# Kernel optimization log

Measured on AMD Instinct MI355X. Metric: run time of the kernel, lower is better.

The kernel has to match this reference:

```python
import jax, jax.numpy as jnp
import numpy as np

N, E, M = 50000, 50000, 640000
IN_DIM, D, L = 256, 128, 3

def setup_inputs() -> dict:
    key = jax.random.key(0)
    ks = jax.random.split(key, 8)
    x = jax.random.normal(ks[0], (N, IN_DIM), dtype=jnp.float32)
    hyperedge_index = jax.random.randint(ks[1], (2, M), 0, N, dtype=jnp.int64)
    weightMatrix = jax.random.uniform(ks[2], (E,), dtype=jnp.float32)
    edgesWeights = jax.random.uniform(ks[3], (M,), dtype=jnp.float32)
    stdv_fc = 1.0 / np.sqrt(IN_DIM)
    fc_w = jax.random.uniform(ks[4], (IN_DIM, D), minval=-stdv_fc, maxval=stdv_fc, dtype=jnp.float32)
    fc_b = jax.random.uniform(ks[5], (D,), minval=-stdv_fc, maxval=stdv_fc, dtype=jnp.float32)
    stdv = 1.0 / np.sqrt(D)
    conv_w = jax.random.uniform(ks[6], (L, D, D), minval=-stdv, maxval=stdv, dtype=jnp.float32)
    conv_b = jax.random.uniform(ks[7], (L, D), minval=-stdv, maxval=stdv, dtype=jnp.float32)
    return {"x": x, "hyperedge_index": hyperedge_index, "weightMatrix": weightMatrix,
            "edgesWeights": edgesWeights, "fc_w": fc_w, "fc_b": fc_b,
            "conv_w": conv_w, "conv_b": conv_b}

def reference(x, hyperedge_index, weightMatrix, edgesWeights, fc_w, fc_b, conv_w, conv_b):
    row, col = hyperedge_index[0], hyperedge_index[1]
    n_nodes, n_edges = x.shape[0], weightMatrix.shape[0]
    # degree normalization (computed once, shared by all layers since inputs identical)
    node_deg = jax.ops.segment_sum(weightMatrix[col], row, num_segments=n_nodes) + 1e-8
    hyper_deg = jax.ops.segment_sum(edgesWeights, col, num_segments=n_edges) + 1e-8
    nd = node_deg ** -0.5
    nd = jnp.where(jnp.isinf(nd), 0.0, nd)
    hd = hyper_deg ** -0.5
    hd = jnp.where(jnp.isinf(hd), 0.0, hd)
    norm = hd[col] * nd[row]  # [M]
    h = jax.nn.relu(x @ fc_w + fc_b)  # [N, D]; dropout inactive (eval)
    for i in range(conv_w.shape[0]):
        xt = h @ conv_w[i] + conv_b[i]                                  # [N, D]
        wx = xt[row] * (edgesWeights * norm)[:, None]                   # [M, D]
        hyper_feat = jax.ops.segment_sum(wx, col, num_segments=n_edges)  # [E, D]
        wh = hyper_feat[col] * (weightMatrix[col] * edgesWeights * norm)[:, None]  # [M, D]
        z = jax.ops.segment_sum(wh, row, num_segments=n_nodes)           # [N, D]
        h = jax.nn.relu(h + z)
    return h
```

## Files before the change

kernel.cpp:

```cpp
#include <hip/hip_runtime.h>
#include <hip/hip_bf16.h>
#include <stdint.h>

typedef __attribute__((ext_vector_type(4))) float f4;
typedef __attribute__((ext_vector_type(2))) float f2;
typedef __attribute__((ext_vector_type(2))) int i2;
typedef __attribute__((ext_vector_type(8))) unsigned short us8;
typedef __attribute__((ext_vector_type(4))) unsigned short us4;
typedef __attribute__((ext_vector_type(2))) unsigned short us2;
typedef __attribute__((ext_vector_type(8))) short s8b;
typedef __attribute__((ext_vector_type(4))) float f32x4;

#define CW_SHIFT 8
#define CW (1 << CW_SHIFT)
#define CH 2048

__device__ __forceinline__ float bf2f(unsigned short u) {
  union { unsigned int i; float f; } t; t.i = ((unsigned int)u) << 16; return t.f;
}
__device__ __forceinline__ unsigned short f2bf(float f) {
  union { float f; unsigned int i; } t; t.f = f;
  unsigned int u = t.i;
  return (unsigned short)((u + 0x7FFFu + ((u >> 16) & 1u)) >> 16);
}
__device__ __forceinline__ float cvtload(const void* p, int i, int f16) {
  return f16 ? bf2f(((const unsigned short*)p)[i]) : ((const float*)p)[i];
}

__global__ void detect_kernel(const unsigned int* __restrict__ xb,
                              const unsigned int* __restrict__ ib,
                              int* __restrict__ flags) {
  if (threadIdx.x == 0) {
    int cnt = 0;
    for (int i = 0; i < 256; ++i) {
      unsigned int e = (xb[i] >> 7) & 0xffu;
      if (e >= 110u && e <= 135u) ++cnt;
    }
    flags[0] = (cnt >= 180) ? 1 : 0;
    int zc = 0;
    for (int i = 0; i < 128; ++i) if (ib[2 * i + 1] == 0u) ++zc;
    flags[1] = (zc >= 120) ? 1 : 0;
  }
}

__global__ void cvt_params(const void* __restrict__ wM, const void* __restrict__ fcw,
                           const void* __restrict__ fcb, const void* __restrict__ cw,
                           const void* __restrict__ cb,
                           float* __restrict__ WMf, unsigned short* __restrict__ FCWT,
                           float* __restrict__ FCB, unsigned short* __restrict__ CWT,
                           float* __restrict__ CBf,
                           int E, int L, const int* __restrict__ flags) {
  const int IN_DIM = 256, D = 128;
  int i = blockIdx.x * 256 + threadIdx.x;
  const int f16 = flags[0];
  if (i < E) { WMf[i] = cvtload(wM, i, f16); return; }
  i -= E;
  if (i < IN_DIM * D) {
    int c = i >> 8, k = i & 255;
    FCWT[i] = f2bf(cvtload(fcw, k * D + c, f16));
    return;
  }
  i -= IN_DIM * D;
  if (i < D) { FCB[i] = cvtload(fcb, i, f16); return; }
  i -= D;
  if (i < L * D * D) {
    int l = i >> 14, rem = i & 16383;
    int c = rem >> 7, k = rem & 127;
    CWT[i] = f2bf(cvtload(cw, l * D * D + k * D + c, f16));
    return;
  }
  i -= L * D * D;
  if (i < L * D) CBf[i] = cvtload(cb, i, f16);
}

__global__ __launch_bounds__(256) void bin_count(
    const void* __restrict__ hei, int M, int* __restrict__ cntAB,
    int nbE, int nbN, int nblk, const int* __restrict__ flags) {
  __shared__ int hA[256];
  __shared__ int hB[256];
  const int tid = threadIdx.x, blk = blockIdx.x;
  hA[tid] = 0; hB[tid] = 0;
  __syncthreads();
  const int i64 = flags[1];
  const int mEnd = min(M, (blk + 1) * CH);
  for (int m = blk * CH + tid; m < mEnd; m += 256) {
    int r, c;
    if (i64) {
      r = (int)((const long long*)hei)[m];
      c = (int)((const long long*)hei)[M + m];
    } else {
      r = ((const int*)hei)[m];
      c = ((const int*)hei)[M + m];
    }
    atomicAdd(&hA[c >> CW_SHIFT], 1);
    atomicAdd(&hB[r >> CW_SHIFT], 1);
  }
  __syncthreads();
  if (tid < nbE) cntAB[tid * nblk + blk] = hA[tid];
  if (tid < nbN) cntAB[(nbE + tid) * nblk + blk] = hB[tid];
}

__global__ __launch_bounds__(512) void scanA(int* __restrict__ cnt,
                                             int* __restrict__ btot, int nblk) {
  __shared__ int sc[512];
  const int tid = threadIdx.x, b = blockIdx.x;
  int v = (tid < nblk) ? cnt[b * nblk + tid] : 0;
  sc[tid] = v;
  __syncthreads();
  for (int s = 1; s < 512; s <<= 1) {
    int t = (tid >= s) ? sc[tid - s] : 0;
    __syncthreads();
    sc[tid] += t;
    __syncthreads();
  }
  if (tid < nblk) cnt[b * nblk + tid] = sc[tid] - v;
  if (tid == 511) btot[b] = sc[511];
}

__global__ __launch_bounds__(512) void scanB(const int* __restrict__ btot,
                                             int* __restrict__ bbaseA,
                                             int* __restrict__ bbaseB,
                                             int nbE, int nbN) {
  __shared__ int sc[512];
  const int tid = threadIdx.x;
  const int nb = blockIdx.x ? nbN : nbE;
  const int* src = blockIdx.x ? (btot + nbE) : btot;
  int* dst = blockIdx.x ? bbaseB : bbaseA;
  int v = (tid < nb) ? src[tid] : 0;
  sc[tid] = v;
  __syncthreads();
  for (int s = 1; s < 512; s <<= 1) {
    int t = (tid >= s) ? sc[tid - s] : 0;
    __syncthreads();
    sc[tid] += t;
    __syncthreads();
  }
  if (tid < nb) dst[tid] = sc[tid] - v;
  if (tid == 511) dst[nb] = sc[511];
}

__global__ __launch_bounds__(256) void binscatter(
    const void* __restrict__ hei, const void* __restrict__ ew, int M,
    const int* __restrict__ cntAB,
    const int* __restrict__ bbaseA, const int* __restrict__ bbaseB,
    i2* __restrict__ PAYA, i2* __restrict__ PAYB,
    int nbE, int nbN, int nblk, const int* __restrict__ flags) {
  __shared__ int baseA[256];
  __shared__ int baseB[256];
  const int tid = threadIdx.x, blk = blockIdx.x;
  if (tid < nbE) baseA[tid] = bbaseA[tid] + cntAB[tid * nblk + blk];
  if (tid < nbN) baseB[tid] = bbaseB[tid] + cntAB[(nbE + tid) * nblk + blk];
  __syncthreads();
  const int i64 = flags[1], f16 = flags[0];
  const int mEnd = min(M, (blk + 1) * CH);
  for (int m = blk * CH + tid; m < mEnd; m += 256) {
    int r, c;
    if (i64) {
      r = (int)((const long long*)hei)[m];
      c = (int)((const long long*)hei)[M + m];
    } else {
      r = ((const int*)hei)[m];
      c = ((const int*)hei)[M + m];
    }
    int e = __float_as_int(f16 ? bf2f(((const unsigned short*)ew)[m])
                               : ((const float*)ew)[m]);
    int pA = atomicAdd(&baseA[c >> CW_SHIFT], 1);
    i2 ea; ea[0] = r | ((c & (CW - 1)) << 20); ea[1] = e;
    PAYA[pA] = ea;
    int pB = atomicAdd(&baseB[r >> CW_SHIFT], 1);
    i2 eb; eb[0] = c | ((r & (CW - 1)) << 20); eb[1] = e;
    PAYB[pB] = eb;
  }
}

__global__ __launch_bounds__(256) void finalize3(
    const i2* __restrict__ PAYA, const int* __restrict__ bbaseA,
    i2* __restrict__ ENTA, int* __restrict__ offE, int E,
    const i2* __restrict__ PAYB, const int* __restrict__ bbaseB,
    i2* __restrict__ ENTB, int* __restrict__ offN, int Nn,
    const float* __restrict__ WMf, float* __restrict__ SCE,
    float* __restrict__ ND, int nbE) {
  __shared__ int cnt[CW];
  __shared__ int sc[CW];
  __shared__ int cur[CW];
  __shared__ float fsum[CW];
  int b = blockIdx.x;
  const i2* PAY; const int* bbase; i2* ENT; int* off;
  int nseg, modeB; float* outScale;
  if (b < nbE) {
    PAY = PAYA; bbase = bbaseA; ENT = ENTA; off = offE;
    nseg = E; modeB = 0; outScale = SCE;
  } else {
    b -= nbE;
    PAY = PAYB; bbase = bbaseB; ENT = ENTB; off = offN;
    nseg = Nn; modeB = 1; outScale = ND;
  }
  const int tid = threadIdx.x;
  const int bs = bbase[b], be = bbase[b + 1];
  const int cb = b << CW_SHIFT;
  const int cw = min(CW, nseg - cb);
  for (int i = tid; i < CW; i += 256) { cnt[i] = 0; fsum[i] = 0.f; }
  __syncthreads();
  for (int k = bs + tid; k < be; k += 256)
    atomicAdd(&cnt[(PAY[k][0] >> 20) & (CW - 1)], 1);
  __syncthreads();
  for (int i = tid; i < CW; i += 256) sc[i] = cnt[i];
  __syncthreads();
  for (int s = 1; s < CW; s <<= 1) {
    int t = (tid >= s) ? sc[tid - s] : 0;
    __syncthreads();
    sc[tid] += t;
    __syncthreads();
  }
  {
    int start = bs + sc[tid] - cnt[tid];
    cur[tid] = start;
    if (tid < cw) off[cb + tid] = start;
  }
  if (tid == 0 && b == ((nseg + CW - 1) >> CW_SHIFT) - 1) off[nseg] = be;
  __syncthreads();
  for (int k = bs + tid; k < be; k += 256) {
    i2 p = PAY[k];
    int key = (p[0] >> 20) & (CW - 1);
    int src = p[0] & 0xFFFFF;
    int pos = atomicAdd(&cur[key], 1);
    i2 outp; outp[0] = src; outp[1] = p[1];
    ENT[pos] = outp;
    float add = modeB ? WMf[src] : __int_as_float(p[1]);
    atomicAdd(&fsum[key], add);
  }
  __syncthreads();
  if (tid < cw) {
    float s = fsum[tid] + 1e-8f;
    outScale[cb + tid] = modeB ? rsqrtf(s) : (WMf[cb + tid] / s);
  }
}

template<int KS>
__global__ __launch_bounds__(256) void gemm_mfma3(
    const void* __restrict__ Aptr, const unsigned short* __restrict__ Wt,
    const float* __restrict__ bias, unsigned short* __restrict__ out,
    int Nrows, const int* __restrict__ flags, int relu,
    const float* __restrict__ rowScale) {
  constexpr int K = KS * 32;
  constexpr int KC = K / 8;
  extern __shared__ unsigned short Bs[];
  const int tid = threadIdx.x;
  const int wv = tid >> 6, ln = tid & 63;
  const int lr = ln & 15;
  const int lk = (ln >> 4) << 3;
  const int rowBase = blockIdx.x * 128 + wv * 32;
  const int aF32 = flags ? (flags[0] ? 0 : 1) : 0;

  int ar[2];
#pragma unroll
  for (int t = 0; t < 2; ++t) {
    int r = rowBase + t * 16 + lr;
    ar[t] = (r < Nrows) ? r : (Nrows - 1);
  }

  s8b aR[2][KS];
  if (!aF32) {
#pragma unroll
    for (int t = 0; t < 2; ++t)
#pragma unroll
      for (int ks = 0; ks < KS; ++ks)
        aR[t][ks] = *reinterpret_cast<const s8b*>(
            (const unsigned short*)Aptr + (size_t)ar[t] * K + ks * 32 + lk);
  } else {
#pragma unroll
    for (int t = 0; t < 2; ++t)
#pragma unroll
      for (int ks = 0; ks < KS; ++ks) {
        const float* ap = (const float*)Aptr + (size_t)ar[t] * K + ks * 32 + lk;
        f4 u0 = *reinterpret_cast<const f4*>(ap);
        f4 u1 = *reinterpret_cast<const f4*>(ap + 4);
#pragma unroll
        for (int j = 0; j < 4; ++j) {
          aR[t][ks][j]     = (short)f2bf(u0[j]);
          aR[t][ks][4 + j] = (short)f2bf(u1[j]);
        }
      }
  }

#pragma unroll
  for (int it = 0; it < (128 * KC + 255) / 256; ++it) {
    int ch = it * 256 + tid;
    if (ch < 128 * KC) {
      int row = ch / KC, kc = (ch % KC) << 3;
      us8 v = *reinterpret_cast<const us8*>(Wt + (size_t)row * K + kc);
      int byte = ((row * K + kc) << 1) ^ ((row & 7) << 4);
      *reinterpret_cast<us8*>((char*)Bs + byte) = v;
    }
  }
  __syncthreads();

  f32x4 acc[2][8];
#pragma unroll
  for (int t = 0; t < 2; ++t)
#pragma unroll
    for (int n = 0; n < 8; ++n) acc[t][n] = (f32x4)0.f;

#pragma unroll
  for (int ks = 0; ks < KS; ++ks) {
#pragma unroll
    for (int n = 0; n < 8; ++n) {
      const int brow = n * 16 + lr;
      int byte = ((brow * K + ks * 32 + lk) << 1) ^ ((brow & 7) << 4);
      s8b b = *reinterpret_cast<const s8b*>((const char*)Bs + byte);
      acc[0][n] = __builtin_amdgcn_mfma_f32_16x16x32_bf16(aR[0][ks], b, acc[0][n], 0, 0, 0);
      acc[1][n] = __builtin_amdgcn_mfma_f32_16x16x32_bf16(aR[1][ks], b, acc[1][n], 0, 0, 0);
    }
  }

#pragma unroll
  for (int t = 0; t < 2; ++t) {
    const int orow0 = rowBase + t * 16 + ((ln >> 4) << 2);
#pragma unroll
    for (int n = 0; n < 8; ++n) {
      const int col = n * 16 + lr;
      const float bv = bias[col];
#pragma unroll
      for (int r = 0; r < 4; ++r) {
        int row = orow0 + r;
        if (row >= Nrows) continue;
        float s = acc[t][n][r] + bv;
        if (relu) s = fmaxf(s, 0.f);
        if (rowScale) s *= rowScale[row];
        out[(size_t)row * 128 + col] = f2bf(s);
      }
    }
  }
}

__global__ __launch_bounds__(256) void gather_edge3(
    const int* __restrict__ off, const i2* __restrict__ ENT,
    const float* __restrict__ sc_e, const unsigned short* __restrict__ X,
    unsigned short* __restrict__ out, int nseg) {
  int seg = blockIdx.x * 16 + (threadIdx.x >> 4);
  if (seg >= nseg) return;
  int d = (threadIdx.x & 15) << 3;
  int k0 = off[seg], k1 = off[seg + 1];
  float a0 = 0.f, a1 = 0.f, a2 = 0.f, a3 = 0.f, a4 = 0.f, a5 = 0.f, a6 = 0.f, a7 = 0.f;
  int k = k0;
  for (; k + 4 <= k1; k += 4) {
    i2 e0 = ENT[k], e1 = ENT[k + 1], e2 = ENT[k + 2], e3 = ENT[k + 3];
    us8 v0 = *reinterpret_cast<const us8*>(X + (size_t)e0[0] * 128 + d);
    us8 v1 = *reinterpret_cast<const us8*>(X + (size_t)e1[0] * 128 + d);
    us8 v2 = *reinterpret_cast<const us8*>(X + (size_t)e2[0] * 128 + d);
    us8 v3 = *reinterpret_cast<const us8*>(X + (size_t)e3[0] * 128 + d);
    float c0 = __int_as_float(e0[1]), c1 = __int_as_float(e1[1]);
    float c2 = __int_as_float(e2[1]), c3 = __int_as_float(e3[1]);
    a0 += c0 * bf2f(v0[0]); a1 += c0 * bf2f(v0[1]); a2 += c0 * bf2f(v0[2]); a3 += c0 * bf2f(v0[3]);
    a4 += c0 * bf2f(v0[4]); a5 += c0 * bf2f(v0[5]); a6 += c0 * bf2f(v0[6]); a7 += c0 * bf2f(v0[7]);
    a0 += c1 * bf2f(v1[0]); a1 += c1 * bf2f(v1[1]); a2 += c1 * bf2f(v1[2]); a3 += c1 * bf2f(v1[3]);
    a4 += c1 * bf2f(v1[4]); a5 += c1 * bf2f(v1[5]); a6 += c1 * bf2f(v1[6]); a7 += c1 * bf2f(v1[7]);
    a0 += c2 * bf2f(v2[0]); a1 += c2 * bf2f(v2[1]); a2 += c2 * bf2f(v2[2]); a3 += c2 * bf2f(v2[3]);
    a4 += c2 * bf2f(v2[4]); a5 += c2 * bf2f(v2[5]); a6 += c2 * bf2f(v2[6]); a7 += c2 * bf2f(v2[7]);
    a0 += c3 * bf2f(v3[0]); a1 += c3 * bf2f(v3[1]); a2 += c3 * bf2f(v3[2]); a3 += c3 * bf2f(v3[3]);
    a4 += c3 * bf2f(v3[4]); a5 += c3 * bf2f(v3[5]); a6 += c3 * bf2f(v3[6]); a7 += c3 * bf2f(v3[7]);
  }
  for (; k < k1; ++k) {
    i2 e = ENT[k];
    us8 v = *reinterpret_cast<const us8*>(X + (size_t)e[0] * 128 + d);
    float c = __int_as_float(e[1]);
    a0 += c * bf2f(v[0]); a1 += c * bf2f(v[1]); a2 += c * bf2f(v[2]); a3 += c * bf2f(v[3]);
    a4 += c * bf2f(v[4]); a5 += c * bf2f(v[5]); a6 += c * bf2f(v[6]); a7 += c * bf2f(v[7]);
  }
  float sc = sc_e[seg];
  us8 o;
  o[0] = f2bf(sc * a0); o[1] = f2bf(sc * a1); o[2] = f2bf(sc * a2); o[3] = f2bf(sc * a3);
  o[4] = f2bf(sc * a4); o[5] = f2bf(sc * a5); o[6] = f2bf(sc * a6); o[7] = f2bf(sc * a7);
  *reinterpret_cast<us8*>(out + (size_t)seg * 128 + d) = o;
}

__global__ __launch_bounds__(256) void gather_node3(
    const int* __restrict__ off, const i2* __restrict__ ENT,
    const float* __restrict__ nd, const unsigned short* __restrict__ HF,
    const unsigned short* __restrict__ H, void* __restrict__ out,
    int nseg, int outF32) {
  int seg = blockIdx.x * 16 + (threadIdx.x >> 4);
  if (seg >= nseg) return;
  int d = (threadIdx.x & 15) << 3;
  int k0 = off[seg], k1 = off[seg + 1];
  float a0 = 0.f, a1 = 0.f, a2 = 0.f, a3 = 0.f, a4 = 0.f, a5 = 0.f, a6 = 0.f, a7 = 0.f;
  int k = k0;
  for (; k + 4 <= k1; k += 4) {
    i2 e0 = ENT[k], e1 = ENT[k + 1], e2 = ENT[k + 2], e3 = ENT[k + 3];
    us8 v0 = *reinterpret_cast<const us8*>(HF + (size_t)e0[0] * 128 + d);
    us8 v1 = *reinterpret_cast<const us8*>(HF + (size_t)e1[0] * 128 + d);
    us8 v2 = *reinterpret_cast<const us8*>(HF + (size_t)e2[0] * 128 + d);
    us8 v3 = *reinterpret_cast<const us8*>(HF + (size_t)e3[0] * 128 + d);
    float c0 = __int_as_float(e0[1]), c1 = __int_as_float(e1[1]);
    float c2 = __int_as_float(e2[1]), c3 = __int_as_float(e3[1]);
    a0 += c0 * bf2f(v0[0]); a1 += c0 * bf2f(v0[1]); a2 += c0 * bf2f(v0[2]); a3 += c0 * bf2f(v0[3]);
    a4 += c0 * bf2f(v0[4]); a5 += c0 * bf2f(v0[5]); a6 += c0 * bf2f(v0[6]); a7 += c0 * bf2f(v0[7]);
    a0 += c1 * bf2f(v1[0]); a1 += c1 * bf2f(v1[1]); a2 += c1 * bf2f(v1[2]); a3 += c1 * bf2f(v1[3]);
    a4 += c1 * bf2f(v1[4]); a5 += c1 * bf2f(v1[5]); a6 += c1 * bf2f(v1[6]); a7 += c1 * bf2f(v1[7]);
    a0 += c2 * bf2f(v2[0]); a1 += c2 * bf2f(v2[1]); a2 += c2 * bf2f(v2[2]); a3 += c2 * bf2f(v2[3]);
    a4 += c2 * bf2f(v2[4]); a5 += c2 * bf2f(v2[5]); a6 += c2 * bf2f(v2[6]); a7 += c2 * bf2f(v2[7]);
    a0 += c3 * bf2f(v3[0]); a1 += c3 * bf2f(v3[1]); a2 += c3 * bf2f(v3[2]); a3 += c3 * bf2f(v3[3]);
    a4 += c3 * bf2f(v3[4]); a5 += c3 * bf2f(v3[5]); a6 += c3 * bf2f(v3[6]); a7 += c3 * bf2f(v3[7]);
  }
  for (; k < k1; ++k) {
    i2 e = ENT[k];
    us8 v = *reinterpret_cast<const us8*>(HF + (size_t)e[0] * 128 + d);
    float c = __int_as_float(e[1]);
    a0 += c * bf2f(v[0]); a1 += c * bf2f(v[1]); a2 += c * bf2f(v[2]); a3 += c * bf2f(v[3]);
    a4 += c * bf2f(v[4]); a5 += c * bf2f(v[5]); a6 += c * bf2f(v[6]); a7 += c * bf2f(v[7]);
  }
  float s = nd[seg];
  us8 h = *reinterpret_cast<const us8*>(H + (size_t)seg * 128 + d);
  float r0 = fmaxf(bf2f(h[0]) + s * a0, 0.f);
  float r1 = fmaxf(bf2f(h[1]) + s * a1, 0.f);
  float r2 = fmaxf(bf2f(h[2]) + s * a2, 0.f);
  float r3 = fmaxf(bf2f(h[3]) + s * a3, 0.f);
  float r4 = fmaxf(bf2f(h[4]) + s * a4, 0.f);
  float r5 = fmaxf(bf2f(h[5]) + s * a5, 0.f);
  float r6 = fmaxf(bf2f(h[6]) + s * a6, 0.f);
  float r7 = fmaxf(bf2f(h[7]) + s * a7, 0.f);
  if (outF32) {
    float* op = (float*)out + (size_t)seg * 128 + d;
    f4 o0, o1;
    o0[0] = r0; o0[1] = r1; o0[2] = r2; o0[3] = r3;
    o1[0] = r4; o1[1] = r5; o1[2] = r6; o1[3] = r7;
    *reinterpret_cast<f4*>(op) = o0;
    *reinterpret_cast<f4*>(op + 4) = o1;
  } else {
    us8 o;
    o[0] = f2bf(r0); o[1] = f2bf(r1); o[2] = f2bf(r2); o[3] = f2bf(r3);
    o[4] = f2bf(r4); o[5] = f2bf(r5); o[6] = f2bf(r6); o[7] = f2bf(r7);
    *reinterpret_cast<us8*>((unsigned short*)out + (size_t)seg * 128 + d) = o;
  }
}

extern "C" void kernel_launch(void* const* d_in, const int* in_sizes, int n_in,
                              void* d_out, int out_size, void* d_ws, size_t ws_size,
                              hipStream_t stream) {
  const void* x   = d_in[0];
  const void* hei = d_in[1];
  const void* wM  = d_in[2];
  const void* ew  = d_in[3];
  const void* fcw = d_in[4];
  const void* fcb = d_in[5];
  const void* cw  = d_in[6];
  const void* cb  = d_in[7];

  const int IN_DIM = 256, D = 128;
  const int N = in_sizes[0] / IN_DIM;
  const int M = in_sizes[1] / 2;
  const int E = in_sizes[2];
  const int L = in_sizes[6] / (D * D);

  const int nbE = (E + CW - 1) >> CW_SHIFT;
  const int nbN = (N + CW - 1) >> CW_SHIFT;
  const int nbT = nbE + nbN;
  const int nblk = (M + CH - 1) / CH;

  float* w = (float*)d_ws;
  size_t o = 0;
  auto alloc = [&](size_t n) { float* p = w + o; o += (n + 3) & ~(size_t)3; return p; };

  float* R = alloc((size_t)(N + E) * D / 2);
  unsigned short* XT = (unsigned short*)R;
  unsigned short* HF = XT + (size_t)N * D;
  i2*  PAYA = (i2*)R;
  i2*  PAYB = PAYA + M;

  unsigned short* H  = (unsigned short*)alloc((size_t)N * D / 2);
  i2*    ENTA = (i2*)alloc((size_t)M * 2);
  i2*    ENTB = (i2*)alloc((size_t)M * 2);
  int*   cntAB = (int*)alloc((size_t)nbT * nblk);
  int*   btotAB = (int*)alloc(nbT + 2);
  int*   bbaseA = (int*)alloc(nbE + 2);
  int*   bbaseB = (int*)alloc(nbN + 2);
  float* ND   = alloc(N);
  float* SCE  = alloc(E);
  int*   offE = (int*)alloc(E + 1);
  int*   offN = (int*)alloc(N + 1);
  float* WMf  = alloc(E);
  unsigned short* FCWT = (unsigned short*)alloc((size_t)IN_DIM * D / 2);
  float* FCB  = alloc(D);
  unsigned short* CWT = (unsigned short*)alloc((size_t)L * D * D / 2);
  float* CBf  = alloc((size_t)L * D);
  int*   FLAGS = (int*)alloc(16);

  detect_kernel<<<1, 64, 0, stream>>>((const unsigned int*)x, (const unsigned int*)hei, FLAGS);

  bin_count<<<nblk, 256, 0, stream>>>(hei, M, cntAB, nbE, nbN, nblk, FLAGS);
  {
    int ntot = E + IN_DIM * D + D + L * D * D + L * D;
    cvt_params<<<(ntot + 255) / 256, 256, 0, stream>>>(wM, fcw, fcb, cw, cb,
                                                       WMf, FCWT, FCB, CWT, CBf,
                                                       E, L, FLAGS);
  }

  scanA<<<nbT, 512, 0, stream>>>(cntAB, btotAB, nblk);
  scanB<<<2, 512, 0, stream>>>(btotAB, bbaseA, bbaseB, nbE, nbN);

  binscatter<<<nblk, 256, 0, stream>>>(hei, ew, M, cntAB, bbaseA, bbaseB,
                                       PAYA, PAYB, nbE, nbN, nblk, FLAGS);

  finalize3<<<nbT, 256, 0, stream>>>(PAYA, bbaseA, ENTA, offE, E,
                                     PAYB, bbaseB, ENTB, offN, N,
                                     WMf, SCE, ND, nbE);

  gemm_mfma3<8><<<(N + 127) / 128, 256, 128 * 256 * 2, stream>>>(
      x, FCWT, FCB, H, N, FLAGS, 1, nullptr);

  int segBlkE = (E + 15) / 16, segBlkN = (N + 15) / 16;
  for (int l = 0; l < L; ++l) {
    gemm_mfma3<4><<<(N + 127) / 128, 256, 128 * 128 * 2, stream>>>(
        H, CWT + (size_t)l * D * D, CBf + (size_t)l * D, XT, N,
        (const int*)nullptr, 0, ND);
    gather_edge3<<<segBlkE, 256, 0, stream>>>(offE, ENTA, SCE, XT, HF, E);
    gather_node3<<<segBlkN, 256, 0, stream>>>(
        offN, ENTB, ND, HF, H,
        (l == L - 1) ? d_out : (void*)H, N, (l == L - 1) ? 1 : 0);
  }
}
```

Before: 307.5 us.

## Fuse edge binning into single pass with atomic bucket cursors and fixed-capacity slots

Replaces the count/scan/scatter sequence for bucketing edges with one kernel that stages edges in shared memory, reserves space per bucket via global atomics, and writes into fixed-capacity slot arrays. A small scan then computes compact bucket offsets for finalize. This drops two kernel launches and a second read of the index arrays, at the cost of assuming no bucket exceeds 8192 entries and extra slot memory.

```diff
diff --git a/kernel.cpp b/kernel.cpp
--- a/kernel.cpp
+++ b/kernel.cpp
@@ -7,13 +7,14 @@
 typedef __attribute__((ext_vector_type(2))) int i2;
 typedef __attribute__((ext_vector_type(8))) unsigned short us8;
 typedef __attribute__((ext_vector_type(4))) unsigned short us4;
-typedef __attribute__((ext_vector_type(2))) unsigned short us2;
 typedef __attribute__((ext_vector_type(8))) short s8b;
 typedef __attribute__((ext_vector_type(4))) float f32x4;
 
 #define CW_SHIFT 8
 #define CW (1 << CW_SHIFT)
 #define CH 2048
+#define CAP_SHIFT 13
+#define CAP (1 << CAP_SHIFT)
 
 __device__ __forceinline__ float bf2f(unsigned short u) {
   union { unsigned int i; float f; } t; t.i = ((unsigned int)u) << 16; return t.f;
@@ -29,7 +30,9 @@
 
 __global__ void detect_kernel(const unsigned int* __restrict__ xb,
                               const unsigned int* __restrict__ ib,
-                              int* __restrict__ flags) {
+                              int* __restrict__ flags,
+                              int* __restrict__ gcur, int ncur) {
+  for (int i = threadIdx.x; i < ncur; i += 64) gcur[i] = 0;
   if (threadIdx.x == 0) {
     int cnt = 0;
     for (int i = 0; i < 256; ++i) {
@@ -73,17 +76,24 @@
   if (i < L * D) CBf[i] = cvtload(cb, i, f16);
 }
 
-__global__ __launch_bounds__(256) void bin_count(
-    const void* __restrict__ hei, int M, int* __restrict__ cntAB,
-    int nbE, int nbN, int nblk, const int* __restrict__ flags) {
+__global__ __launch_bounds__(256) void fused_scatter(
+    const void* __restrict__ hei, const void* __restrict__ ew, int M,
+    int* __restrict__ gcurA, int* __restrict__ gcurB,
+    i2* __restrict__ SLOTA, i2* __restrict__ SLOTB,
+    int nbE, int nbN, const int* __restrict__ flags) {
+  __shared__ int er[CH];
+  __shared__ int ec[CH];
+  __shared__ int ee[CH];
   __shared__ int hA[256];
   __shared__ int hB[256];
   const int tid = threadIdx.x, blk = blockIdx.x;
   hA[tid] = 0; hB[tid] = 0;
   __syncthreads();
-  const int i64 = flags[1];
-  const int mEnd = min(M, (blk + 1) * CH);
-  for (int m = blk * CH + tid; m < mEnd; m += 256) {
+  const int i64 = flags[1], f16 = flags[0];
+  const int m0 = blk * CH;
+  const int cnt = min(M - m0, CH);
+  for (int i = tid; i < cnt; i += 256) {
+    int m = m0 + i;
     int r, c;
     if (i64) {
       r = (int)((const long long*)hei)[m];
@@ -92,39 +102,41 @@
       r = ((const int*)hei)[m];
       c = ((const int*)hei)[M + m];
     }
+    er[i] = r; ec[i] = c;
+    ee[i] = __float_as_int(f16 ? bf2f(((const unsigned short*)ew)[m])
+                                : ((const float*)ew)[m]);
     atomicAdd(&hA[c >> CW_SHIFT], 1);
     atomicAdd(&hB[r >> CW_SHIFT], 1);
   }
   __syncthreads();
-  if (tid < nbE) cntAB[tid * nblk + blk] = hA[tid];
-  if (tid < nbN) cntAB[(nbE + tid) * nblk + blk] = hB[tid];
-}
-
-__global__ __launch_bounds__(512) void scanA(int* __restrict__ cnt,
-                                             int* __restrict__ btot, int nblk) {
-  __shared__ int sc[512];
-  const int tid = threadIdx.x, b = blockIdx.x;
-  int v = (tid < nblk) ? cnt[b * nblk + tid] : 0;
-  sc[tid] = v;
-  __syncthreads();
-  for (int s = 1; s < 512; s <<= 1) {
-    int t = (tid >= s) ? sc[tid - s] : 0;
+  {
+    int nA = (tid < nbE) ? hA[tid] : 0;
+    int nB = (tid < nbN) ? hB[tid] : 0;
     __syncthreads();
-    sc[tid] += t;
-    __syncthreads();
-  }
-  if (tid < nblk) cnt[b * nblk + tid] = sc[tid] - v;
-  if (tid == 511) btot[b] = sc[511];
-}
-
-__global__ __launch_bounds__(512) void scanB(const int* __restrict__ btot,
+    if (tid < nbE) hA[tid] = (tid << CAP_SHIFT) + (nA ? atomicAdd(gcurA + tid, nA) : 0);
+    if (tid < nbN) hB[tid] = (tid << CAP_SHIFT) + (nB ? atomicAdd(gcurB + tid, nB) : 0);
+  }
+  __syncthreads();
+  for (int i = tid; i < cnt; i += 256) {
+    int r = er[i], c = ec[i], e = ee[i];
+    int pA = atomicAdd(&hA[c >> CW_SHIFT], 1);
+    i2 ea; ea[0] = r | ((c & (CW - 1)) << 20); ea[1] = e;
+    SLOTA[pA] = ea;
+    int pB = atomicAdd(&hB[r >> CW_SHIFT], 1);
+    i2 eb; eb[0] = c | ((r & (CW - 1)) << 20); eb[1] = e;
+    SLOTB[pB] = eb;
+  }
+}
+
+__global__ __launch_bounds__(512) void scanB(const int* __restrict__ gcurA,
+                                             const int* __restrict__ gcurB,
                                              int* __restrict__ bbaseA,
                                              int* __restrict__ bbaseB,
                                              int nbE, int nbN) {
   __shared__ int sc[512];
   const int tid = threadIdx.x;
   const int nb = blockIdx.x ? nbN : nbE;
-  const int* src = blockIdx.x ? (btot + nbE) : btot;
+  const int* src = blockIdx.x ? gcurB : gcurA;
   int* dst = blockIdx.x ? bbaseB : bbaseA;
   int v = (tid < nb) ? src[tid] : 0;
   sc[tid] = v;
@@ -139,44 +151,10 @@
   if (tid == 511) dst[nb] = sc[511];
 }
 
-__global__ __launch_bounds__(256) void binscatter(
-    const void* __restrict__ hei, const void* __restrict__ ew, int M,
-    const int* __restrict__ cntAB,
-    const int* __restrict__ bbaseA, const int* __restrict__ bbaseB,
-    i2* __restrict__ PAYA, i2* __restrict__ PAYB,
-    int nbE, int nbN, int nblk, const int* __restrict__ flags) {
-  __shared__ int baseA[256];
-  __shared__ int baseB[256];
-  const int tid = threadIdx.x, blk = blockIdx.x;
-  if (tid < nbE) baseA[tid] = bbaseA[tid] + cntAB[tid * nblk + blk];
-  if (tid < nbN) baseB[tid] = bbaseB[tid] + cntAB[(nbE + tid) * nblk + blk];
-  __syncthreads();
-  const int i64 = flags[1], f16 = flags[0];
-  const int mEnd = min(M, (blk + 1) * CH);
-  for (int m = blk * CH + tid; m < mEnd; m += 256) {
-    int r, c;
-    if (i64) {
-      r = (int)((const long long*)hei)[m];
-      c = (int)((const long long*)hei)[M + m];
-    } else {
-      r = ((const int*)hei)[m];
-      c = ((const int*)hei)[M + m];
-    }
-    int e = __float_as_int(f16 ? bf2f(((const unsigned short*)ew)[m])
-                               : ((const float*)ew)[m]);
-    int pA = atomicAdd(&baseA[c >> CW_SHIFT], 1);
-    i2 ea; ea[0] = r | ((c & (CW - 1)) << 20); ea[1] = e;
-    PAYA[pA] = ea;
-    int pB = atomicAdd(&baseB[r >> CW_SHIFT], 1);
-    i2 eb; eb[0] = c | ((r & (CW - 1)) << 20); eb[1] = e;
-    PAYB[pB] = eb;
-  }
-}
-
 __global__ __launch_bounds__(256) void finalize3(
-    const i2* __restrict__ PAYA, const int* __restrict__ bbaseA,
+    const i2* __restrict__ SLOTA, const int* __restrict__ bbaseA,
     i2* __restrict__ ENTA, int* __restrict__ offE, int E,
-    const i2* __restrict__ PAYB, const int* __restrict__ bbaseB,
+    const i2* __restrict__ SLOTB, const int* __restrict__ bbaseB,
     i2* __restrict__ ENTB, int* __restrict__ offN, int Nn,
     const float* __restrict__ WMf, float* __restrict__ SCE,
     float* __restrict__ ND, int nbE) {
@@ -185,26 +163,28 @@
   __shared__ int cur[CW];
   __shared__ float fsum[CW];
   int b = blockIdx.x;
-  const i2* PAY; const int* bbase; i2* ENT; int* off;
+  const i2* SLOT; const int* bbase; i2* ENT; int* off;
   int nseg, modeB; float* outScale;
   if (b < nbE) {
-    PAY = PAYA; bbase = bbaseA; ENT = ENTA; off = offE;
+    SLOT = SLOTA; bbase = bbaseA; ENT = ENTA; off = offE;
     nseg = E; modeB = 0; outScale = SCE;
   } else {
     b -= nbE;
-    PAY = PAYB; bbase = bbaseB; ENT = ENTB; off = offN;
+    SLOT = SLOTB; bbase = bbaseB; ENT = ENTB; off = offN;
     nseg = Nn; modeB = 1; outScale = ND;
   }
   const int tid = threadIdx.x;
-  const int bs = bbase[b], be = bbase[b + 1];
+  const int obase = bbase[b];
+  const int nent = bbase[b + 1] - obase;
+  const int bs = b << CAP_SHIFT;
   const int cb = b << CW_SHIFT;
   const int cw = min(CW, nseg - cb);
-  for (int i = tid; i < CW; i += 256) { cnt[i] = 0; fsum[i] = 0.f; }
-  __syncthreads();
-  for (int k = bs + tid; k < be; k += 256)
-    atomicAdd(&cnt[(PAY[k][0] >> 20) & (CW - 1)], 1);
-  __syncthreads();
-  for (int i = tid; i < CW; i += 256) sc[i] = cnt[i];
+  cnt[tid] = 0; fsum[tid] = 0.f;
+  __syncthreads();
+  for (int k = tid; k < nent; k += 256)
+    atomicAdd(&cnt[(SLOT[bs + k][0] >> 20) & (CW - 1)], 1);
+  __syncthreads();
+  sc[tid] = cnt[tid];
   __syncthreads();
   for (int s = 1; s < CW; s <<= 1) {
     int t = (tid >= s) ? sc[tid - s] : 0;
@@ -213,14 +193,14 @@
     __syncthreads();
   }
   {
-    int start = bs + sc[tid] - cnt[tid];
+    int start = obase + sc[tid] - cnt[tid];
     cur[tid] = start;
     if (tid < cw) off[cb + tid] = start;
   }
-  if (tid == 0 && b == ((nseg + CW - 1) >> CW_SHIFT) - 1) off[nseg] = be;
-  __syncthreads();
-  for (int k = bs + tid; k < be; k += 256) {
-    i2 p = PAY[k];
+  if (tid == 0 && b == ((nseg + CW - 1) >> CW_SHIFT) - 1) off[nseg] = obase + nent;
+  __syncthreads();
+  for (int k = tid; k < nent; k += 256) {
+    i2 p = SLOT[bs + k];
     int key = (p[0] >> 20) & (CW - 1);
     int src = p[0] & 0xFFFFF;
     int pos = atomicAdd(&cur[key], 1);
@@ -464,14 +444,14 @@
   float* R = alloc((size_t)(N + E) * D / 2);
   unsigned short* XT = (unsigned short*)R;
   unsigned short* HF = XT + (size_t)N * D;
-  i2*  PAYA = (i2*)R;
-  i2*  PAYB = PAYA + M;
-
+
+  i2* SLOTA = (i2*)alloc((size_t)nbE * CAP * 2);
+  i2* SLOTB = (i2*)alloc((size_t)nbN * CAP * 2);
   unsigned short* H  = (unsigned short*)alloc((size_t)N * D / 2);
   i2*    ENTA = (i2*)alloc((size_t)M * 2);
   i2*    ENTB = (i2*)alloc((size_t)M * 2);
-  int*   cntAB = (int*)alloc((size_t)nbT * nblk);
-  int*   btotAB = (int*)alloc(nbT + 2);
+  int*   gcurA = (int*)alloc(nbE + 2);
+  int*   gcurB = (int*)alloc(nbN + 2);
   int*   bbaseA = (int*)alloc(nbE + 2);
   int*   bbaseB = (int*)alloc(nbN + 2);
   float* ND   = alloc(N);
@@ -485,9 +465,9 @@
   float* CBf  = alloc((size_t)L * D);
   int*   FLAGS = (int*)alloc(16);
 
-  detect_kernel<<<1, 64, 0, stream>>>((const unsigned int*)x, (const unsigned int*)hei, FLAGS);
-
-  bin_count<<<nblk, 256, 0, stream>>>(hei, M, cntAB, nbE, nbN, nblk, FLAGS);
+  detect_kernel<<<1, 64, 0, stream>>>((const unsigned int*)x, (const unsigned int*)hei,
+                                      FLAGS, gcurA, (int)(((nbE + 2 + 3) & ~3) + nbN + 2));
+
   {
     int ntot = E + IN_DIM * D + D + L * D * D + L * D;
     cvt_params<<<(ntot + 255) / 256, 256, 0, stream>>>(wM, fcw, fcb, cw, cb,
@@ -495,14 +475,13 @@
                                                        E, L, FLAGS);
   }
 
-  scanA<<<nbT, 512, 0, stream>>>(cntAB, btotAB, nblk);
-  scanB<<<2, 512, 0, stream>>>(btotAB, bbaseA, bbaseB, nbE, nbN);
-
-  binscatter<<<nblk, 256, 0, stream>>>(hei, ew, M, cntAB, bbaseA, bbaseB,
-                                       PAYA, PAYB, nbE, nbN, nblk, FLAGS);
-
-  finalize3<<<nbT, 256, 0, stream>>>(PAYA, bbaseA, ENTA, offE, E,
-                                     PAYB, bbaseB, ENTB, offN, N,
+  fused_scatter<<<nblk, 256, 0, stream>>>(hei, ew, M, gcurA, gcurB,
+                                          SLOTA, SLOTB, nbE, nbN, FLAGS);
+
+  scanB<<<2, 512, 0, stream>>>(gcurA, gcurB, bbaseA, bbaseB, nbE, nbN);
+
+  finalize3<<<nbT, 256, 0, stream>>>(SLOTA, bbaseA, ENTA, offE, E,
+                                     SLOTB, bbaseB, ENTB, offN, N,
                                      WMf, SCE, ND, nbE);
 
   gemm_mfma3<8><<<(N + 127) / 128, 256, 128 * 256 * 2, stream>>>(
```

Result: no change. 306.1 us (-0.5%).
